# Optimization experiments

Hardware: AMD Instinct MI355X
Metric: run time of the kernel (lower is better)

The kernel has to match this reference:

```python
import jax, jax.numpy as jnp
import numpy as np

NEG = jnp.float32(-1e9)  # -inf surrogate, safe for logsumexp
EPS = 1e-7               # keras.backend.epsilon()


def _ctc_loss(y_true, y_pred):
    """Faithful K.ctc_batch_cost with full input/label lengths.

    y_true: [B, L] int labels in [0, C-2] (blank = C-1, TF convention)
    y_pred: [B, T, C] softmax probabilities
    returns: [B, 1] negative log-likelihood per sample
    """
    B, T, C = y_pred.shape
    L = y_true.shape[1]
    blank = C - 1
    S = 2 * L + 1  # extended label: blank-interleaved

    logp = jnp.log(y_pred + EPS)  # [B, T, C]

    # Extended label sequence [blank, l1, blank, l2, ..., lL, blank]
    ext = jnp.full((B, S), blank, dtype=jnp.int32).at[:, 1::2].set(
        y_true.astype(jnp.int32))  # [B, S]

    # Skip transition (s-2 -> s) allowed iff ext[s] != blank and ext[s] != ext[s-2]
    skip = jnp.concatenate(
        [jnp.zeros((B, 2), dtype=bool),
         (ext[:, 2:] != blank) & (ext[:, 2:] != ext[:, :-2])],
        axis=1)  # [B, S]

    # Gather lattice log-probs once: [B, T, S]
    lp = jnp.take_along_axis(logp, ext[:, None, :], axis=2)

    # alpha at t=0: only states 0 (blank) and 1 (first label) reachable
    alpha0 = jnp.full((B, S), NEG).at[:, 0].set(lp[:, 0, 0]).at[:, 1].set(lp[:, 0, 1])

    def step(alpha, lp_t):
        a1 = alpha                                                     # stay
        a2 = jnp.pad(alpha[:, :-1], ((0, 0), (1, 0)), constant_values=NEG)  # advance 1
        a3 = jnp.pad(alpha[:, :-2], ((0, 0), (2, 0)), constant_values=NEG)  # advance 2
        a3 = jnp.where(skip, a3, NEG)
        new = lp_t + jax.nn.logsumexp(jnp.stack([a1, a2, a3]), axis=0)
        return new, None

    lp_rest = jnp.transpose(lp[:, 1:, :], (1, 0, 2))  # [T-1, B, S]
    alphaT, _ = jax.lax.scan(step, alpha0, lp_rest)

    # Total log-prob ends in last blank or last label
    ll = jax.nn.logsumexp(alphaT[:, S - 2:S], axis=1)  # [B]
    return -ll[:, None]  # [B, 1], matches ctc_batch_cost's expand_dims


def setup_inputs() -> dict:
    key = jax.random.key(0)
    k1, k2 = jax.random.split(key)
    B, T, C, L = 512, 512, 128, 64
    logits = jax.random.normal(k1, (B, T, C), dtype=jnp.float32)
    y_pred = jax.nn.softmax(logits, axis=-1)  # ctc_batch_cost expects probs
    y_true = jax.random.randint(k2, (B, L), 0, C - 1)  # labels exclude blank C-1
    return {"y_true": y_true, "y_pred": y_pred}


def reference(y_true, y_pred):
    return _ctc_loss(y_true, y_pred)
```

## Files before the change

kernel.cpp:

```cpp
#include <hip/hip_runtime.h>


constexpr int Tn = 512;
constexpr int Cn = 128;
constexpr int Ln = 64;
constexpr float NEGF = -1e9f;
constexpr float EPSF = 1e-7f;
constexpr float LN2F = 0.6931471805599453f;

#define EXP2F(x) __builtin_amdgcn_exp2f(x)
#define LOG2F(x) __builtin_amdgcn_logf(x)

__device__ __forceinline__ float dpp_shr1(float x) {
    return __int_as_float(__builtin_amdgcn_update_dpp(
        0, __float_as_int(x), 0x138 , 0xF, 0xF, true));
}

__global__ __launch_bounds__(64)
void ctc_fwd(const int* __restrict__ y_true,
             const float* __restrict__ y_pred,
             float* __restrict__ out)
{
    const int b    = blockIdx.x;
    const int lane = threadIdx.x;

    const float2* __restrict__ row = (const float2*)(y_pred + (size_t)b * Tn * Cn);

    const int  lab   = y_true[b * Ln + lane];
    const int  labp  = __shfl_up(lab, 1, 64);
    const bool skip  = (lane > 0) && (lab != labp);
    const int  baddr = (lab >> 1) << 2;
    const bool bhi   = (lab & 1) != 0;
    const bool l0    = (lane == 0);

    float2 pv[16];
    float  bpLo[4], bpHi[4];
    float  lpLv[4];
    float  lpbv[8];

    float aA, aB, aZ;

    float2 p0 = row[lane];
    #pragma unroll
    for (int k = 0; k < 16; ++k) pv[k] = row[(1 + k) * 64 + lane];

    {
        float g0 = LOG2F(p0.x + EPSF);
        float g1 = LOG2F(p0.y + EPSF);
        aZ = __int_as_float(__builtin_amdgcn_readlane(__float_as_int(g1), 63));
        float bl = __int_as_float(__builtin_amdgcn_ds_bpermute(baddr, __float_as_int(g0)));
        float bh = __int_as_float(__builtin_amdgcn_ds_bpermute(baddr, __float_as_int(g1)));
        float lpl0 = bhi ? bh : bl;
        aA = l0 ? lpl0 : NEGF;
        aB = NEGF;
    }

    #pragma unroll
    for (int j = 0; j < 8; ++j) {
        float g0 = LOG2F(pv[j].x + EPSF);
        float g1 = LOG2F(pv[j].y + EPSF);
        lpbv[j] = __int_as_float(__builtin_amdgcn_readlane(__float_as_int(g1), 63));
        float bl = __int_as_float(__builtin_amdgcn_ds_bpermute(baddr, __float_as_int(g0)));
        float bh = __int_as_float(__builtin_amdgcn_ds_bpermute(baddr, __float_as_int(g1)));
        if (j < 4) lpLv[j] = bhi ? bh : bl;
        else { bpLo[j - 4] = bl; bpHi[j - 4] = bh; }
    }

    auto consume = [&](int u) {
        float lpb = lpbv[u & 7];
        float lpl = lpLv[u & 3];
        float upA = dpp_shr1(aA);
        float upB = dpp_shr1(aB);
        upA = l0 ? NEGF : upA;
        upB = l0 ? aZ   : upB;
        float a3 = skip ? upA : NEGF;
        float m1 = fmaxf(fmaxf(aA, upB), a3);
        float s1 = EXP2F(aA - m1) + EXP2F(upB - m1) + EXP2F(a3 - m1);
        float nA = lpl + m1 + LOG2F(s1);
        float m2 = fmaxf(aB, aA);
        float n2 = fminf(aB, aA);
        float nB = lpb + m2 + LOG2F(1.0f + EXP2F(n2 - m2));
        aZ += lpb;
        aA = nA; aB = nB;
    };
    auto stageB = [&](int u) {
        lpLv[u & 3] = bhi ? bpHi[u & 3] : bpLo[u & 3];
    };
    auto stageA = [&](int u) {
        float2 p = pv[(u + 8) & 15];
        float g0 = LOG2F(p.x + EPSF);
        float g1 = LOG2F(p.y + EPSF);
        lpbv[u & 7] = __int_as_float(__builtin_amdgcn_readlane(__float_as_int(g1), 63));
        bpLo[u & 3] = __int_as_float(__builtin_amdgcn_ds_bpermute(baddr, __float_as_int(g0)));
        bpHi[u & 3] = __int_as_float(__builtin_amdgcn_ds_bpermute(baddr, __float_as_int(g1)));
    };

    int t = 1;
    for (int blk = 0; blk < 31; ++blk) {
        #pragma unroll
        for (int u = 0; u < 16; ++u, ++t) {
            consume(u);
            stageB(u);
            stageA(u);
            int rn = t + 16; rn = rn > 511 ? 511 : rn;
            pv[u] = row[rn * 64 + lane];
        }
    }
    #pragma unroll
    for (int u = 0; u < 15; ++u, ++t) {
        consume(u);
        stageB(u);
        stageA(u);
    }

    float m  = fmaxf(aA, aB);
    float n  = fminf(aA, aB);
    float ll = m + LOG2F(1.0f + EXP2F(n - m));
    if (lane == 63) out[b] = -ll * LN2F;
}

extern "C" void kernel_launch(void* const* d_in, const int* in_sizes, int n_in,
                              void* d_out, int out_size, void* d_ws, size_t ws_size,
                              hipStream_t stream)
{
    const int*   y_true = (const int*)d_in[0];
    const float* y_pred = (const float*)d_in[1];
    float*       out    = (float*)d_out;

    const int B = out_size;
    ctc_fwd<<<dim3(B), dim3(64), 0, stream>>>(y_true, y_pred, out);
}
```

Before: 210.9 us.

## Deepen prefetch ring to 32 steps and take log after lane permute

The per-timestep prefetch ring grows from 16 to 32 float2 registers, so global loads are issued further ahead of use. Log2 is now applied only to the two values each lane actually consumes (the gathered label prob and the lane-63 blank prob), after the bpermute/readlane, instead of to both raw probabilities before gathering. This cuts the number of transcendentals per step and hides more memory latency. The costs are more register pressure and a wrapping load index that issues a few redundant reloads.

Result: faster. 200.1 us (-5.1%).

```diff
diff --git a/kernel.cpp b/kernel.cpp
--- a/kernel.cpp
+++ b/kernel.cpp
@@ -1,9 +1,6 @@
 #include <hip/hip_runtime.h>
 
 
-constexpr int Tn = 512;
-constexpr int Cn = 128;
-constexpr int Ln = 64;
 constexpr float NEGF = -1e9f;
 constexpr float EPSF = 1e-7f;
 constexpr float LN2F = 0.6931471805599453f;
@@ -15,6 +12,12 @@
     return __int_as_float(__builtin_amdgcn_update_dpp(
         0, __float_as_int(x), 0x138 , 0xF, 0xF, true));
 }
+__device__ __forceinline__ float bperm(int addr, float x) {
+    return __int_as_float(__builtin_amdgcn_ds_bpermute(addr, __float_as_int(x)));
+}
+__device__ __forceinline__ float rdl63(float x) {
+    return __int_as_float(__builtin_amdgcn_readlane(__float_as_int(x), 63));
+}
 
 __global__ __launch_bounds__(64)
 void ctc_fwd(const int* __restrict__ y_true,
@@ -24,50 +27,51 @@
     const int b    = blockIdx.x;
     const int lane = threadIdx.x;
 
-    const float2* __restrict__ row = (const float2*)(y_pred + (size_t)b * Tn * Cn);
+    const float2* __restrict__ rowp =
+        (const float2*)(y_pred + (size_t)b * 512 * 128) + lane;
 
-    const int  lab   = y_true[b * Ln + lane];
+    const int  lab   = y_true[b * 64 + lane];
     const int  labp  = __shfl_up(lab, 1, 64);
     const bool skip  = (lane > 0) && (lab != labp);
     const int  baddr = (lab >> 1) << 2;
     const bool bhi   = (lab & 1) != 0;
     const bool l0    = (lane == 0);
 
-    float2 pv[16];
+    float2 pv[32];
     float  bpLo[4], bpHi[4];
-    float  lpLv[4];
-    float  lpbv[8];
+    float  lpLv[4], lpbv[4];
+    float  aA, aB, aZ;
 
-    float aA, aB, aZ;
-
-    float2 p0 = row[lane];
+    float2 p0 = rowp[0];
     #pragma unroll
-    for (int k = 0; k < 16; ++k) pv[k] = row[(1 + k) * 64 + lane];
+    for (int r = 1; r <= 32; ++r) pv[r & 31] = rowp[r * 64];
 
     {
-        float g0 = LOG2F(p0.x + EPSF);
-        float g1 = LOG2F(p0.y + EPSF);
-        aZ = __int_as_float(__builtin_amdgcn_readlane(__float_as_int(g1), 63));
-        float bl = __int_as_float(__builtin_amdgcn_ds_bpermute(baddr, __float_as_int(g0)));
-        float bh = __int_as_float(__builtin_amdgcn_ds_bpermute(baddr, __float_as_int(g1)));
-        float lpl0 = bhi ? bh : bl;
-        aA = l0 ? lpl0 : NEGF;
+        float blo = bperm(baddr, p0.x);
+        float bh  = bperm(baddr, p0.y);
+        float pl  = bhi ? bh : blo;
+        aZ = LOG2F(rdl63(p0.y) + EPSF);
+        aA = l0 ? LOG2F(pl + EPSF) : NEGF;
         aB = NEGF;
     }
-
     #pragma unroll
-    for (int j = 0; j < 8; ++j) {
-        float g0 = LOG2F(pv[j].x + EPSF);
-        float g1 = LOG2F(pv[j].y + EPSF);
-        lpbv[j] = __int_as_float(__builtin_amdgcn_readlane(__float_as_int(g1), 63));
-        float bl = __int_as_float(__builtin_amdgcn_ds_bpermute(baddr, __float_as_int(g0)));
-        float bh = __int_as_float(__builtin_amdgcn_ds_bpermute(baddr, __float_as_int(g1)));
-        if (j < 4) lpLv[j] = bhi ? bh : bl;
-        else { bpLo[j - 4] = bl; bpHi[j - 4] = bh; }
+    for (int r = 1; r <= 4; ++r) {
+        float2 p  = pv[r & 31];
+        float blo = bperm(baddr, p.x);
+        float bh  = bperm(baddr, p.y);
+        float pl  = bhi ? bh : blo;
+        lpLv[r & 3] = LOG2F(pl + EPSF);
+        lpbv[r & 3] = LOG2F(rdl63(p.y) + EPSF);
+    }
+    #pragma unroll
+    for (int r = 5; r <= 8; ++r) {
+        float2 p = pv[r & 31];
+        bpLo[r & 3] = bperm(baddr, p.x);
+        bpHi[r & 3] = bperm(baddr, p.y);
     }
 
-    auto consume = [&](int u) {
-        float lpb = lpbv[u & 7];
+    auto slot = [&](int t, int u, bool doLoad) {
+        float lpb = lpbv[u & 3];
         float lpl = lpLv[u & 3];
         float upA = dpp_shr1(aA);
         float upB = dpp_shr1(aB);
@@ -82,35 +86,32 @@
         float nB = lpb + m2 + LOG2F(1.0f + EXP2F(n2 - m2));
         aZ += lpb;
         aA = nA; aB = nB;
-    };
-    auto stageB = [&](int u) {
-        lpLv[u & 3] = bhi ? bpHi[u & 3] : bpLo[u & 3];
-    };
-    auto stageA = [&](int u) {
-        float2 p = pv[(u + 8) & 15];
-        float g0 = LOG2F(p.x + EPSF);
-        float g1 = LOG2F(p.y + EPSF);
-        lpbv[u & 7] = __int_as_float(__builtin_amdgcn_readlane(__float_as_int(g1), 63));
-        bpLo[u & 3] = __int_as_float(__builtin_amdgcn_ds_bpermute(baddr, __float_as_int(g0)));
-        bpHi[u & 3] = __int_as_float(__builtin_amdgcn_ds_bpermute(baddr, __float_as_int(g1)));
+        {
+            int q = (u + 4) & 3;
+            float pl = bhi ? bpHi[q] : bpLo[q];
+            lpLv[q] = LOG2F(pl + EPSF);
+            lpbv[q] = LOG2F(rdl63(pv[(u + 4) & 31].y) + EPSF);
+        }
+        {
+            int q = (u + 8) & 3;
+            float2 p = pv[(u + 8) & 31];
+            bpLo[q] = bperm(baddr, p.x);
+            bpHi[q] = bperm(baddr, p.y);
+        }
+        if (doLoad) pv[u] = rowp[((t + 32) & 511) * 64];
     };
 
-    int t = 1;
-    for (int blk = 0; blk < 31; ++blk) {
+    for (int blk = 0; blk < 15; ++blk) {
+        int t0 = 1 + blk * 32;
         #pragma unroll
-        for (int u = 0; u < 16; ++u, ++t) {
-            consume(u);
-            stageB(u);
-            stageA(u);
-            int rn = t + 16; rn = rn > 511 ? 511 : rn;
-            pv[u] = row[rn * 64 + lane];
-        }
+        for (int i = 0; i < 32; ++i)
+            slot(t0 + i, (1 + i) & 31, true);
     }
-    #pragma unroll
-    for (int u = 0; u < 15; ++u, ++t) {
-        consume(u);
-        stageB(u);
-        stageA(u);
+    {
+        int t0 = 481;
+        #pragma unroll
+        for (int i = 0; i < 31; ++i)
+            slot(t0 + i, (1 + i) & 31, false);
     }
 
     float m  = fmaxf(aA, aB);
```
